# Performance work log

Measured on AMD Instinct MI355X. Metric: run time of the kernel, lower is better.

The kernel has to match this reference:

```python
import jax, jax.numpy as jnp
import numpy as np

ALPHA = 0.2  # LeakyReLU negative slope
NEG_INF = -1e9


def setup_inputs() -> dict:
    key = jax.random.key(0)
    k1, k2, k3, k4 = jax.random.split(key, 4)
    B, N, Fin, Fout = 8, 2048, 128, 64
    h = jax.random.normal(k1, (B, N, Fin), dtype=jnp.float32)
    adj_mask = jax.random.randint(k2, (B, N, N), 0, 2).astype(jnp.int32)
    # xavier_uniform-style scales
    W = jax.random.uniform(k3, (Fout, Fin), dtype=jnp.float32,
                           minval=-1.0, maxval=1.0) * np.sqrt(6.0 / (Fin + Fout))
    a = jax.random.uniform(k4, (2 * Fout,), dtype=jnp.float32,
                           minval=-1.0, maxval=1.0) * np.sqrt(6.0 / (2 * Fout + 1))
    return {"h": h, "adj_mask": adj_mask, "W": W, "a": a}


def reference(h, adj_mask, W, a):
    # Wh: [B, N, Fout]
    Wh = jnp.einsum("bnf,of->bno", h, W)
    Fout = Wh.shape[-1]
    a1, a2 = a[:Fout], a[Fout:]
    # additive decomposition of a([Wh_i || Wh_j]): e_ij = leakyrelu(s1_i + s2_j)
    s1 = Wh @ a1  # [B, N]
    s2 = Wh @ a2  # [B, N]
    e = jax.nn.leaky_relu(s1[:, :, None] + s2[:, None, :], negative_slope=ALPHA)  # [B,N,N]
    e = jnp.where(adj_mask == 0, NEG_INF, e)
    attention = jax.nn.softmax(e, axis=-1)
    # dropout is identity in eval mode / p effectively 0 for the reference
    h_prime = jnp.einsum("bij,bjo->bio", attention, Wh)
    return h_prime
```

## Files before the change

### kernel.cpp

```cpp
#include <hip/hip_runtime.h>
#include <hip/hip_fp16.h>
#include <math.h>

#define LRELU_ALPHA 0.2f
#define NEG_INF -1000000000.0f
#define L2E 1.44269504088896340736f

constexpr int B_ = 8, N_ = 2048, FIN = 128, FOUT = 64;

typedef _Float16 __attribute__((ext_vector_type(8))) f16x8;
typedef float __attribute__((ext_vector_type(4))) f32x4;

__device__ __forceinline__ void gload16(const void* g, void* l) {
  __builtin_amdgcn_global_load_lds(
      (const __attribute__((address_space(1))) void*)g,
      (__attribute__((address_space(3))) void*)l, 16, 0, 0);
}

__global__ __launch_bounds__(256) void k_wh(
    const float* __restrict__ h, const float* __restrict__ W,
    const float* __restrict__ a, unsigned short* __restrict__ WhT,
    float* __restrict__ s1, float* __restrict__ s2) {
  __shared__ float Wt[128][65];
  __shared__ float hs[16][128];

  const int t = threadIdx.x;
  const int row0 = blockIdx.x * 16;

  for (int e = t; e < 64 * 128; e += 256) {
    int o = e >> 7, f = e & 127;
    Wt[f][o] = W[e];
  }
  {
    const float4* hg = (const float4*)(h + (size_t)row0 * FIN);
    for (int i4 = t; i4 < 16 * 32; i4 += 256) {
      int r = i4 >> 5, f4 = i4 & 31;
      *(float4*)&hs[r][f4 * 4] = hg[i4];
    }
  }
  __syncthreads();

  const int wave = t >> 6, lane = t & 63;
  float acc[4] = {0.f, 0.f, 0.f, 0.f};
#pragma unroll 4
  for (int f4 = 0; f4 < 32; ++f4) {
    float w0 = Wt[4 * f4 + 0][lane], w1 = Wt[4 * f4 + 1][lane];
    float w2 = Wt[4 * f4 + 2][lane], w3 = Wt[4 * f4 + 3][lane];
#pragma unroll
    for (int r = 0; r < 4; ++r) {
      float4 hv = *(const float4*)&hs[wave * 4 + r][f4 * 4];
      acc[r] += hv.x * w0 + hv.y * w1 + hv.z * w2 + hv.w * w3;
    }
  }

  const float a1v = a[lane], a2v = a[64 + lane];
  const int b = row0 / N_;
#pragma unroll
  for (int r = 0; r < 4; ++r) {
    const int row = row0 + wave * 4 + r;
    const int n = row - b * N_;
    const float v = acc[r];
    WhT[((size_t)b * 64 + lane) * N_ + n] = __half_as_ushort(__float2half(v));
    float p1 = v * a1v, p2 = v * a2v;
#pragma unroll
    for (int d = 32; d; d >>= 1) {
      p1 += __shfl_xor(p1, d, 64);
      p2 += __shfl_xor(p2, d, 64);
    }
    if (lane == 0) { s1[row] = p1; s2[row] = p2; }
  }
}

__global__ __launch_bounds__(256, 4) void k_attn(
    const unsigned short* __restrict__ WhT,
    const float* __restrict__ s1g, const float* __restrict__ s2g,
    const int* __restrict__ adj, float* __restrict__ out) {
  __shared__ __align__(16) unsigned char sbuf[2][12 * 1024];
  __shared__ float s2s[N_];

  const int t = threadIdx.x;
  const int wave = t >> 6, lane = t & 63;
  const int m = lane & 15, q = lane >> 4;
  const int b = blockIdx.x;
  const int i0 = blockIdx.y * 16;

  const int* adjB = adj + (size_t)b * N_ * N_;
  const unsigned short* whB = WhT + (size_t)b * 64 * N_;

  {
    const float4* s2R = (const float4*)(s2g + (size_t)b * N_);
    for (int i = t; i < N_ / 4; i += 256) {
      float4 v = s2R[i];
      v.x *= L2E; v.y *= L2E; v.z *= L2E; v.w *= L2E;
      ((float4*)s2s)[i] = v;
    }
  }

  const float s1r = s1g[b * N_ + i0 + m];
  const float c1 = (s1r - 2.0f) * L2E;
  const float c2 = (LRELU_ALPHA * s1r - 2.0f) * L2E;

  f16x8 ones;
#pragma unroll
  for (int j = 0; j < 8; ++j) ones[j] = (_Float16)1.0f;

  const unsigned char* gp[3];
  int gs[3];
#pragma unroll
  for (int s = 0; s < 3; ++s) {
    const int j = wave * 3 + s;
    if (j < 4) {
      const int ks = j >> 1, hh = j & 1;
      gp[s] = (const unsigned char*)(adjB + (size_t)(i0 + m) * N_ +
                                     ks * 32 + q * 8 + hh * 4);
      gs[s] = 64 * 4;
    } else {
      const int g = (j - 4) >> 1, ks = (j - 4) & 1;
      gp[s] = (const unsigned char*)(whB + (size_t)(g * 16 + m) * N_ +
                                     ks * 32 + q * 8);
      gs[s] = 64 * 2;
    }
  }

#define STAGE(S, c)                                                         \
  {                                                                         \
    _Pragma("unroll") for (int s = 0; s < 3; ++s)                           \
        gload16(gp[s] + (size_t)(c) * gs[s],                                \
                (S) + (wave * 3 + s) * 1024 + lane * 16);                   \
  }

  f32x4 acc = {0.f, 0.f, 0.f, 0.f}, accS = acc;

  auto consume = [&](const unsigned char* base, int c) {
#pragma unroll
    for (int ks = 0; ks < 2; ++ks) {
      int4 A0 = *(const int4*)(base + (ks * 2 + 0) * 1024 + lane * 16);
      int4 A1 = *(const int4*)(base + (ks * 2 + 1) * 1024 + lane * 16);
      const float* sp = &s2s[c * 64 + ks * 32 + q * 8];
      float4 sv0 = *(const float4*)sp;
      float4 sv1 = *(const float4*)(sp + 4);
      float xs[8] = {sv0.x, sv0.y, sv0.z, sv0.w, sv1.x, sv1.y, sv1.z, sv1.w};
      int avs[8] = {A0.x, A0.y, A0.z, A0.w, A1.x, A1.y, A1.z, A1.w};
      f16x8 af;
#pragma unroll
      for (int j = 0; j < 8; ++j) {
        float x = xs[j];
        float e = fmaxf(c1 + x, fmaf(LRELU_ALPHA, x, c2));
        e = avs[j] ? e : NEG_INF;
        af[j] = (_Float16)__builtin_amdgcn_exp2f(e);
      }
      f16x8 bf =
          *(const f16x8*)(base + (4 + wave * 2 + ks) * 1024 + lane * 16);
      acc = __builtin_amdgcn_mfma_f32_16x16x32_f16(af, bf, acc, 0, 0, 0);
      accS = __builtin_amdgcn_mfma_f32_16x16x32_f16(af, ones, accS, 0, 0, 0);
    }
  };

  STAGE(sbuf[0], 0)
  STAGE(sbuf[1], 1)
  __syncthreads();

  for (int c = 0; c < 30; ++c) {
    consume(sbuf[c & 1], c);
    __builtin_amdgcn_s_barrier();
    STAGE(sbuf[c & 1], c + 2)
    asm volatile("s_waitcnt vmcnt(3)" ::: "memory");
    __builtin_amdgcn_s_barrier();
  }
  consume(sbuf[0], 30);
  asm volatile("s_waitcnt vmcnt(0)" ::: "memory");
  __builtin_amdgcn_s_barrier();
  consume(sbuf[1], 31);

#pragma unroll
  for (int r = 0; r < 4; ++r) {
    const float l = accS[r];
    const float inv = (l == 0.f) ? 1.f : 1.f / l;
    const size_t row = (size_t)b * N_ + i0 + q * 4 + r;
    out[row * FOUT + wave * 16 + m] = acc[r] * inv;
  }
#undef STAGE
}

extern "C" void kernel_launch(void* const* d_in, const int* in_sizes, int n_in,
                              void* d_out, int out_size, void* d_ws, size_t ws_size,
                              hipStream_t stream) {
  const float* h   = (const float*)d_in[0];
  const int*   adj = (const int*)d_in[1];
  const float* W   = (const float*)d_in[2];
  const float* a   = (const float*)d_in[3];
  float* out = (float*)d_out;

  unsigned short* WhT = (unsigned short*)d_ws;
  float* s1 = (float*)(WhT + (size_t)B_ * 64 * N_);
  float* s2 = s1 + (size_t)B_ * N_;

  k_wh<<<dim3(B_ * N_ / 16), 256, 0, stream>>>(h, W, a, WhT, s1, s2);
  k_attn<<<dim3(B_, N_ / 16), 256, 0, stream>>>(WhT, s1, s2, adj, out);
}
```

Measured before the change: 236.5 us.

## Split key dimension across waves with per-wave pipelines and LDS reduction

The attention kernel now gives each wave its own 512-column slice of the key dimension instead of one 16-column output slice. Each wave computes the exp scores once per chunk and feeds four MFMAs covering all 64 output features, so no exp work is repeated across waves. Adjacency values are loaded straight into registers and Wh goes through per-wave LDS buffers, which removes the block-wide barriers from the main loop. The cost is a final cross-wave reduction through LDS, plus larger LDS use and more accumulator registers, which may lower occupancy.

```diff
diff --git a/kernel.cpp b/kernel.cpp
--- a/kernel.cpp
+++ b/kernel.cpp
@@ -75,7 +75,7 @@
     const unsigned short* __restrict__ WhT,
     const float* __restrict__ s1g, const float* __restrict__ s2g,
     const int* __restrict__ adj, float* __restrict__ out) {
-  __shared__ __align__(16) unsigned char sbuf[2][12 * 1024];
+  __shared__ __align__(16) unsigned char sbuf[2][16 * 1024];
   __shared__ float s2s[N_];
 
   const int t = threadIdx.x;
@@ -83,9 +83,7 @@
   const int m = lane & 15, q = lane >> 4;
   const int b = blockIdx.x;
   const int i0 = blockIdx.y * 16;
-
-  const int* adjB = adj + (size_t)b * N_ * N_;
-  const unsigned short* whB = WhT + (size_t)b * 64 * N_;
+  const int jw = wave * 512;
 
   {
     const float4* s2R = (const float4*)(s2g + (size_t)b * N_);
@@ -104,82 +102,107 @@
 #pragma unroll
   for (int j = 0; j < 8; ++j) ones[j] = (_Float16)1.0f;
 
-  const unsigned char* gp[3];
-  int gs[3];
-#pragma unroll
-  for (int s = 0; s < 3; ++s) {
-    const int j = wave * 3 + s;
-    if (j < 4) {
-      const int ks = j >> 1, hh = j & 1;
-      gp[s] = (const unsigned char*)(adjB + (size_t)(i0 + m) * N_ +
-                                     ks * 32 + q * 8 + hh * 4);
-      gs[s] = 64 * 4;
-    } else {
-      const int g = (j - 4) >> 1, ks = (j - 4) & 1;
-      gp[s] = (const unsigned char*)(whB + (size_t)(g * 16 + m) * N_ +
-                                     ks * 32 + q * 8);
-      gs[s] = 64 * 2;
-    }
-  }
-
-#define STAGE(S, c)                                                         \
-  {                                                                         \
-    _Pragma("unroll") for (int s = 0; s < 3; ++s)                           \
-        gload16(gp[s] + (size_t)(c) * gs[s],                                \
-                (S) + (wave * 3 + s) * 1024 + lane * 16);                   \
-  }
-
-  f32x4 acc = {0.f, 0.f, 0.f, 0.f}, accS = acc;
-
-  auto consume = [&](const unsigned char* base, int c) {
-#pragma unroll
-    for (int ks = 0; ks < 2; ++ks) {
-      int4 A0 = *(const int4*)(base + (ks * 2 + 0) * 1024 + lane * 16);
-      int4 A1 = *(const int4*)(base + (ks * 2 + 1) * 1024 + lane * 16);
-      const float* sp = &s2s[c * 64 + ks * 32 + q * 8];
-      float4 sv0 = *(const float4*)sp;
-      float4 sv1 = *(const float4*)(sp + 4);
-      float xs[8] = {sv0.x, sv0.y, sv0.z, sv0.w, sv1.x, sv1.y, sv1.z, sv1.w};
-      int avs[8] = {A0.x, A0.y, A0.z, A0.w, A1.x, A1.y, A1.z, A1.w};
-      f16x8 af;
-#pragma unroll
-      for (int j = 0; j < 8; ++j) {
-        float x = xs[j];
-        float e = fmaxf(c1 + x, fmaf(LRELU_ALPHA, x, c2));
-        e = avs[j] ? e : NEG_INF;
-        af[j] = (_Float16)__builtin_amdgcn_exp2f(e);
-      }
-      f16x8 bf =
-          *(const f16x8*)(base + (4 + wave * 2 + ks) * 1024 + lane * 16);
-      acc = __builtin_amdgcn_mfma_f32_16x16x32_f16(af, bf, acc, 0, 0, 0);
-      accS = __builtin_amdgcn_mfma_f32_16x16x32_f16(af, ones, accS, 0, 0, 0);
-    }
-  };
-
-  STAGE(sbuf[0], 0)
-  STAGE(sbuf[1], 1)
+  const int* adjR =
+      adj + (size_t)b * N_ * N_ + (size_t)(i0 + m) * N_ + jw + q * 8;
+  const unsigned short* whL =
+      WhT + (size_t)b * 64 * N_ + (size_t)m * N_ + jw + q * 8;
+
+  unsigned char* d0 = sbuf[0] + wave * 4096;
+  unsigned char* d1 = sbuf[1] + wave * 4096;
+
+#define STAGE(D, c)                                                       \
+  {                                                                       \
+    _Pragma("unroll") for (int g = 0; g < 4; ++g)                         \
+        gload16(whL + (size_t)g * 16 * N_ + (c) * 32, (D) + g * 1024);    \
+  }
+#define ISSUE(R0, R1, c)                                 \
+  {                                                      \
+    const int4* ap = (const int4*)(adjR + (c) * 32);     \
+    R0 = ap[0];                                          \
+    R1 = ap[1];                                          \
+  }
+#define CONSUME(R0, R1, D, c)                                                \
+  {                                                                          \
+    const float* sp = &s2s[jw + (c) * 32 + q * 8];                           \
+    float4 sv0 = *(const float4*)sp;                                         \
+    float4 sv1 = *(const float4*)(sp + 4);                                   \
+    float xs[8] = {sv0.x, sv0.y, sv0.z, sv0.w, sv1.x, sv1.y, sv1.z, sv1.w};  \
+    int avs[8] = {R0.x, R0.y, R0.z, R0.w, R1.x, R1.y, R1.z, R1.w};           \
+    f16x8 af;                                                                \
+    _Pragma("unroll") for (int j = 0; j < 8; ++j) {                          \
+      float x = xs[j];                                                       \
+      float e = fmaxf(c1 + x, fmaf(LRELU_ALPHA, x, c2));                     \
+      e = avs[j] ? e : NEG_INF;                                              \
+      af[j] = (_Float16)__builtin_amdgcn_exp2f(e);  \
+    }                                                                        \
+    f16x8 bf0 = *(const f16x8*)((D) + 0 * 1024 + lane * 16);                 \
+    f16x8 bf1 = *(const f16x8*)((D) + 1 * 1024 + lane * 16);                 \
+    f16x8 bf2 = *(const f16x8*)((D) + 2 * 1024 + lane * 16);                 \
+    f16x8 bf3 = *(const f16x8*)((D) + 3 * 1024 + lane * 16);                 \
+    acc0 = __builtin_amdgcn_mfma_f32_16x16x32_f16(af, bf0, acc0, 0, 0, 0);   \
+    acc1 = __builtin_amdgcn_mfma_f32_16x16x32_f16(af, bf1, acc1, 0, 0, 0);   \
+    acc2 = __builtin_amdgcn_mfma_f32_16x16x32_f16(af, bf2, acc2, 0, 0, 0);   \
+    acc3 = __builtin_amdgcn_mfma_f32_16x16x32_f16(af, bf3, acc3, 0, 0, 0);   \
+    accS = __builtin_amdgcn_mfma_f32_16x16x32_f16(af, ones, accS, 0, 0, 0);  \
+  }
+#define FV(NN) asm volatile("s_waitcnt vmcnt(" #NN ")" ::: "memory");
+#define FL() asm volatile("s_waitcnt lgkmcnt(0)" ::: "memory");
+
+  int4 rA0, rA1, rB0, rB1;
+  f32x4 acc0 = {0.f, 0.f, 0.f, 0.f}, acc1 = acc0, acc2 = acc0, acc3 = acc0,
+        accS = acc0;
+
   __syncthreads();
 
-  for (int c = 0; c < 30; ++c) {
-    consume(sbuf[c & 1], c);
-    __builtin_amdgcn_s_barrier();
-    STAGE(sbuf[c & 1], c + 2)
-    asm volatile("s_waitcnt vmcnt(3)" ::: "memory");
-    __builtin_amdgcn_s_barrier();
-  }
-  consume(sbuf[0], 30);
-  asm volatile("s_waitcnt vmcnt(0)" ::: "memory");
-  __builtin_amdgcn_s_barrier();
-  consume(sbuf[1], 31);
-
-#pragma unroll
-  for (int r = 0; r < 4; ++r) {
-    const float l = accS[r];
+  ISSUE(rA0, rA1, 0) STAGE(d0, 0)
+  ISSUE(rB0, rB1, 1) STAGE(d1, 1)
+
+  for (int c = 0; c < 14; c += 2) {
+    FV(6) CONSUME(rA0, rA1, d0, c)
+    FL() ISSUE(rA0, rA1, c + 2) STAGE(d0, c + 2)
+    FV(6) CONSUME(rB0, rB1, d1, c + 1)
+    FL() ISSUE(rB0, rB1, c + 3) STAGE(d1, c + 3)
+  }
+  FV(6) CONSUME(rA0, rA1, d0, 14)
+  FV(0) CONSUME(rB0, rB1, d1, 15)
+
+  {
+    float* redw = (float*)d0;
+#pragma unroll
+    for (int r = 0; r < 4; ++r) {
+      redw[(q * 4 + r) * 64 + 0 * 16 + m] = acc0[r];
+      redw[(q * 4 + r) * 64 + 1 * 16 + m] = acc1[r];
+      redw[(q * 4 + r) * 64 + 2 * 16 + m] = acc2[r];
+      redw[(q * 4 + r) * 64 + 3 * 16 + m] = acc3[r];
+    }
+    if (m == 0) {
+      float* redSw = (float*)d1;
+#pragma unroll
+      for (int r = 0; r < 4; ++r) redSw[q * 4 + r] = accS[r];
+    }
+  }
+  __syncthreads();
+
+  {
+    const int row = t >> 4, c4 = t & 15;
+    float4 v = {0.f, 0.f, 0.f, 0.f};
+    float l = 0.f;
+#pragma unroll
+    for (int w2 = 0; w2 < 4; ++w2) {
+      float4 pv = ((const float4*)(sbuf[0] + w2 * 4096))[row * 16 + c4];
+      v.x += pv.x; v.y += pv.y; v.z += pv.z; v.w += pv.w;
+      l += ((const float*)(sbuf[1] + w2 * 4096))[row];
+    }
     const float inv = (l == 0.f) ? 1.f : 1.f / l;
-    const size_t row = (size_t)b * N_ + i0 + q * 4 + r;
-    out[row * FOUT + wave * 16 + m] = acc[r] * inv;
+    float4 o;
+    o.x = v.x * inv; o.y = v.y * inv; o.z = v.z * inv; o.w = v.w * inv;
+    ((float4*)(out + ((size_t)b * N_ + i0 + row) * FOUT))[c4] = o;
   }
 #undef STAGE
+#undef ISSUE
+#undef CONSUME
+#undef FV
+#undef FL
 }
 
 extern "C" void kernel_launch(void* const* d_in, const int* in_sizes, int n_in,
```

Measured after the change: 237.0 us. No clear change (+0.2%).
